# Kernel optimization log

Measured on AMD Instinct MI355X. Metric: run time of the kernel, lower is better.

The kernel has to match this reference:

```python
import jax, jax.numpy as jnp
import numpy as np

N_NODES = 50000
N_EDGES = 800000
IN_DIM = 128
HIDDEN = 128
NUM_CLASSES = 2
NUM_GRAPHS = 512


def _linear_params(key, fan_in, fan_out):
    # torch nn.Linear default init: U(-1/sqrt(fan_in), 1/sqrt(fan_in))
    k1, k2 = jax.random.split(key)
    bound = 1.0 / np.sqrt(fan_in)
    W = jax.random.uniform(k1, (fan_in, fan_out), jnp.float32, -bound, bound)
    b = jax.random.uniform(k2, (fan_out,), jnp.float32, -bound, bound)
    return W, b


def setup_inputs() -> dict:
    key = jax.random.key(0)
    ks = jax.random.split(key, 8)
    x = jax.random.normal(ks[0], (N_NODES, IN_DIM), jnp.float32)
    edge_index = jax.random.randint(ks[1], (2, N_EDGES), 0, N_NODES, jnp.int64)
    batch = jnp.sort(jax.random.randint(ks[2], (N_NODES,), 0, NUM_GRAPHS, jnp.int64))
    W1a, b1a = _linear_params(ks[3], IN_DIM, HIDDEN)
    W1b, b1b = _linear_params(ks[4], HIDDEN, HIDDEN)
    W2a, b2a = _linear_params(ks[5], HIDDEN, HIDDEN)
    W2b, b2b = _linear_params(ks[6], HIDDEN, HIDDEN)
    Wfc, bfc = _linear_params(ks[7], HIDDEN, NUM_CLASSES)
    return {"x": x, "edge_index": edge_index, "batch": batch,
            "W1a": W1a, "b1a": b1a, "W1b": W1b, "b1b": b1b,
            "W2a": W2a, "b2a": b2a, "W2b": W2b, "b2b": b2b,
            "Wfc": Wfc, "bfc": bfc}


def _gin_layer(x, src, dst, Wa, ba, Wb, bb):
    # GINConv (eps=0): h_i = MLP(x_i + sum_{j->i} x_j)
    agg = jax.ops.segment_sum(x[src], dst, num_segments=N_NODES)
    h = x + agg
    h = jax.nn.relu(h @ Wa + ba)
    h = h @ Wb + bb
    return jax.nn.relu(h)  # outer F.relu in forward; dropout is identity (eval)


def reference(x, edge_index, batch, W1a, b1a, W1b, b1b, W2a, b2a, W2b, b2b, Wfc, bfc):
    src, dst = edge_index[0], edge_index[1]
    h = _gin_layer(x, src, dst, W1a, b1a, W1b, b1b)
    h = _gin_layer(h, src, dst, W2a, b2a, W2b, b2b)
    # global mean pool per graph
    sums = jax.ops.segment_sum(h, batch, num_segments=NUM_GRAPHS)
    counts = jax.ops.segment_sum(jnp.ones((N_NODES,), h.dtype), batch, num_segments=NUM_GRAPHS)
    g_emb = sums / jnp.maximum(counts, 1.0)[:, None]
    return g_emb @ Wfc + bfc  # [NUM_GRAPHS, NUM_CLASSES]
```

## Files before the change

### kernel.cpp

```cpp
#include <hip/hip_runtime.h>

typedef unsigned short ushort_t;
typedef unsigned int uint_t;

typedef __bf16 bf16x8 __attribute__((ext_vector_type(8)));
typedef float f32x4 __attribute__((ext_vector_type(4)));

#define N_NODES 50000
#define N_EDGES 800000
#define DIM 128
#define NUM_GRAPHS 512
#define LDA 136

#define ELL_CAP 64

#define EDGE_GROUPS 8
#define EDGE_BUCKET ((N_NODES + EDGE_GROUPS - 1) / EDGE_GROUPS)
#define A_CHUNK 2048
#define A_BLOCKS ((N_EDGES + A_CHUNK - 1) / A_CHUNK)
#define FIFO_CAP 110592

#define PREP_X_BLOCKS 6250
#define PREP_W_BLOCKS 256
#define PREP_B_BLOCKS 196
#define PREP_TOTAL (A_BLOCKS + PREP_X_BLOCKS + PREP_W_BLOCKS + PREP_B_BLOCKS + 1)

#define SCATTER_BLOCKS 512

__device__ __forceinline__ float bf2f(ushort_t u) {
    return __uint_as_float(((uint_t)u) << 16);
}
__device__ __forceinline__ ushort_t f2bf(float f) {
    uint_t u = __float_as_uint(f);
    u = (u + 0x7FFF + ((u >> 16) & 1)) >> 16;
    return (ushort_t)u;
}
__device__ __forceinline__ bf16x8 as_bf16x8(uint4 v) {
    return __builtin_bit_cast(bf16x8, v);
}

__global__ void zero_detect_kernel(int* cnt, float* gsum, int* gcnt, const void* xraw,
                                   const void* eiraw, int* flags) {
    int i = blockIdx.x * 256 + threadIdx.x;
    if (i < N_NODES) cnt[i] = 0;
    if (i < NUM_GRAPHS * DIM) gsum[i] = 0.f;
    if (i < EDGE_GROUPS) gcnt[i] = 0;
    if (i == 0) {
        const ushort_t* u = (const ushort_t*)xraw;
        int extreme = 0;
        for (int k = 0; k < 128; ++k) {
            int e = (u[k] >> 7) & 0xFF;
            if (e >= 0xC0) extreme++;
        }
        flags[0] = (extreme > 8) ? 1 : 0;
        const int* p = (const int*)eiraw;
        int nonzero = 0;
        for (int k = 1; k < 64; k += 2) nonzero += (p[k] != 0);
        flags[1] = (nonzero == 0) ? 1 : 0;
    }
}

__global__ __launch_bounds__(256) void prep_all_kernel(
    const void* xraw, const void* braw, const void* eiraw,
    const void* W0, const void* W1, const void* W2, const void* W3,
    const void* pb1a, const void* pb1b, const void* pb2a, const void* pb2b,
    const void* pWfc, const void* pbfc, const int* __restrict__ flags,
    ushort_t* __restrict__ xout, ushort_t* __restrict__ wpout,
    int* __restrict__ batch32, float* __restrict__ params,
    int* __restrict__ gcnt, int2* __restrict__ fifo) {
    __shared__ int lcnt[EDGE_GROUPS];
    __shared__ int lbase[EDGE_GROUPS];
    int b = blockIdx.x;
    int tid = threadIdx.x;
    if (b < A_BLOCKS) {
        if (tid < EDGE_GROUPS) lcnt[tid] = 0;
        __syncthreads();
        const int* p = (const int*)eiraw;
        int i64 = flags[1];
        int base_e = b * A_CHUNK;
        int g[8], r[8], sv[8], dv[8];
#pragma unroll
        for (int k = 0; k < 8; ++k) {
            int e = base_e + k * 256 + tid;
            int valid = e < N_EDGES;
            int s = 0, d = 0;
            if (valid) {
                if (i64) { s = p[2 * e]; d = p[2 * (N_EDGES + e)]; }
                else     { s = p[e];     d = p[N_EDGES + e]; }
            }
            sv[k] = s; dv[k] = d;
            g[k] = valid ? (d / EDGE_BUCKET) : -1;
            r[k] = 0;
            if (valid) r[k] = atomicAdd(&lcnt[g[k]], 1);
        }
        __syncthreads();
        if (tid < EDGE_GROUPS) lbase[tid] = atomicAdd(&gcnt[tid], lcnt[tid]);
        __syncthreads();
#pragma unroll
        for (int k = 0; k < 8; ++k) {
            if (g[k] >= 0) {
                int pos = lbase[g[k]] + r[k];
                if (pos < FIFO_CAP)
                    fifo[(size_t)g[k] * FIFO_CAP + pos] = make_int2(sv[k], dv[k]);
            }
        }
    } else if (b < A_BLOCKS + PREP_X_BLOCKS) {
        if (flags[0]) {
            int i = (b - A_BLOCKS) * 256 + tid;
            if (i < N_NODES * DIM / 4) {
                float4 v = ((const float4*)xraw)[i];
                ushort4 o;
                o.x = f2bf(v.x); o.y = f2bf(v.y); o.z = f2bf(v.z); o.w = f2bf(v.w);
                ((ushort4*)xout)[i] = o;
            }
        }
    } else if (b < A_BLOCKS + PREP_X_BLOCKS + PREP_W_BLOCKS) {
        int gidx = (b - A_BLOCKS - PREP_X_BLOCKS) * 256 + tid;
        int which = gidx >> 14;
        const void* W = (which == 0) ? W0 : (which == 1) ? W1 : (which == 2) ? W2 : W3;
        int idx = gidx & 16383;
        int j = idx & 7;
        int L = (idx >> 3) & 63;
        int t = (idx >> 9) & 7;
        int s = idx >> 12;
        int k = s * 32 + (L >> 4) * 8 + j;
        int n = t * 16 + (L & 15);
        int off = k * DIM + n;
        wpout[gidx] = flags[0] ? f2bf(((const float*)W)[off]) : ((const ushort_t*)W)[off];
    } else if (b < A_BLOCKS + PREP_X_BLOCKS + PREP_W_BLOCKS + PREP_B_BLOCKS) {
        int i = (b - A_BLOCKS - PREP_X_BLOCKS - PREP_W_BLOCKS) * 256 + tid;
        if (i < N_NODES) {
            const int* p = (const int*)braw;
            batch32[i] = flags[1] ? p[2 * i] : p[i];
        }
    } else {
        for (int i = tid; i < 770; i += 256) {
            const void* srcp;
            int j;
            if (i < 128)      { srcp = pb1a; j = i; }
            else if (i < 256) { srcp = pb1b; j = i - 128; }
            else if (i < 384) { srcp = pb2a; j = i - 256; }
            else if (i < 512) { srcp = pb2b; j = i - 384; }
            else if (i < 768) { srcp = pWfc; j = i - 512; }
            else              { srcp = pbfc; j = i - 768; }
            params[i] = flags[0] ? ((const float*)srcp)[j] : bf2f(((const ushort_t*)srcp)[j]);
        }
    }
}

__global__ __launch_bounds__(256) void scatter_kernel(const int2* __restrict__ fifo,
                                                      const int* __restrict__ gcnt,
                                                      int* __restrict__ cnt,
                                                      int* __restrict__ ell) {
    int g = blockIdx.x & (EDGE_GROUPS - 1);
    int sub = blockIdx.x >> 3;
    int n = gcnt[g];
    if (n > FIFO_CAP) n = FIFO_CAP;
    const int2* f = fifo + (size_t)g * FIFO_CAP;
    for (int i = sub * 256 + threadIdx.x; i < n; i += (SCATTER_BLOCKS / EDGE_GROUPS) * 256) {
        int2 sd = f[i];
        int slot = atomicAdd(&cnt[sd.y], 1);
        if (slot < ELL_CAP) ell[sd.y * ELL_CAP + slot] = sd.x;
    }
}

__global__ __launch_bounds__(256) void agg_kernel(const ushort_t* __restrict__ featA,
                                                  const void* __restrict__ featB,
                                                  const int* __restrict__ flags,
                                                  const int* __restrict__ deg,
                                                  const int* __restrict__ ell,
                                                  ushort_t* __restrict__ hout) {
    int n = blockIdx.x * 16 + (threadIdx.x >> 4);
    int lane = threadIdx.x & 15;
    if (n >= N_NODES) return;
    const ushort_t* feat = featA;
    if (flags && !flags[0]) feat = (const ushort_t*)featB;
    const uint4* fp = reinterpret_cast<const uint4*>(feat);
    uint4 v = fp[(size_t)n * 16 + lane];
    float a0 = bf2f((ushort_t)(v.x & 0xffff));
    float a1 = bf2f((ushort_t)(v.x >> 16));
    float a2 = bf2f((ushort_t)(v.y & 0xffff));
    float a3 = bf2f((ushort_t)(v.y >> 16));
    float a4 = bf2f((ushort_t)(v.z & 0xffff));
    float a5 = bf2f((ushort_t)(v.z >> 16));
    float a6 = bf2f((ushort_t)(v.w & 0xffff));
    float a7 = bf2f((ushort_t)(v.w >> 16));
    int e1 = deg[n];
    if (e1 > ELL_CAP) e1 = ELL_CAP;
    const int4* __restrict__ rp4 = reinterpret_cast<const int4*>(ell + (size_t)n * ELL_CAP);
    const int* __restrict__ row = ell + (size_t)n * ELL_CAP;
    int j = 0;
#define ACC8(V) \
    a0 += bf2f((ushort_t)((V).x & 0xffff)); a1 += bf2f((ushort_t)((V).x >> 16)); \
    a2 += bf2f((ushort_t)((V).y & 0xffff)); a3 += bf2f((ushort_t)((V).y >> 16)); \
    a4 += bf2f((ushort_t)((V).z & 0xffff)); a5 += bf2f((ushort_t)((V).z >> 16)); \
    a6 += bf2f((ushort_t)((V).w & 0xffff)); a7 += bf2f((ushort_t)((V).w >> 16));
    for (; j + 8 <= e1; j += 8) {
        int4 ra = rp4[j >> 2];
        int4 rb = rp4[(j >> 2) + 1];
        uint4 g0 = fp[(size_t)ra.x * 16 + lane];
        uint4 g1 = fp[(size_t)ra.y * 16 + lane];
        uint4 g2 = fp[(size_t)ra.z * 16 + lane];
        uint4 g3 = fp[(size_t)ra.w * 16 + lane];
        uint4 g4 = fp[(size_t)rb.x * 16 + lane];
        uint4 g5 = fp[(size_t)rb.y * 16 + lane];
        uint4 g6 = fp[(size_t)rb.z * 16 + lane];
        uint4 g7 = fp[(size_t)rb.w * 16 + lane];
        ACC8(g0) ACC8(g1) ACC8(g2) ACC8(g3)
        ACC8(g4) ACC8(g5) ACC8(g6) ACC8(g7)
    }
    for (; j + 4 <= e1; j += 4) {
        int4 ra = rp4[j >> 2];
        uint4 g0 = fp[(size_t)ra.x * 16 + lane];
        uint4 g1 = fp[(size_t)ra.y * 16 + lane];
        uint4 g2 = fp[(size_t)ra.z * 16 + lane];
        uint4 g3 = fp[(size_t)ra.w * 16 + lane];
        ACC8(g0) ACC8(g1) ACC8(g2) ACC8(g3)
    }
    for (; j < e1; ++j) {
        int s = row[j];
        uint4 g0 = fp[(size_t)s * 16 + lane];
        ACC8(g0)
    }
#undef ACC8
    uint4 o;
    o.x = (uint_t)f2bf(a0) | ((uint_t)f2bf(a1) << 16);
    o.y = (uint_t)f2bf(a2) | ((uint_t)f2bf(a3) << 16);
    o.z = (uint_t)f2bf(a4) | ((uint_t)f2bf(a5) << 16);
    o.w = (uint_t)f2bf(a6) | ((uint_t)f2bf(a7) << 16);
    reinterpret_cast<uint4*>(hout)[(size_t)n * 16 + lane] = o;
}

__global__ __launch_bounds__(256) void mlp_kernel(const ushort_t* __restrict__ hin,
                                                  const ushort_t* __restrict__ wpA,
                                                  const float* __restrict__ ba,
                                                  const ushort_t* __restrict__ wpB,
                                                  const float* __restrict__ bb,
                                                  ushort_t* __restrict__ hout) {
    __shared__ ushort_t As[64 * LDA];
    int tid = threadIdx.x;
    int wave = tid >> 6;
    int lane = tid & 63;
    int quad = lane >> 4;
    int cl = lane & 15;
    int row0 = blockIdx.x * 64;

    bf16x8 B1[2][4], B2[2][4];
#pragma unroll
    for (int ti = 0; ti < 2; ++ti) {
        int t = 2 * wave + ti;
#pragma unroll
        for (int s = 0; s < 4; ++s) {
            B1[ti][s] = as_bf16x8(reinterpret_cast<const uint4*>(wpA)[(s * 8 + t) * 64 + lane]);
            B2[ti][s] = as_bf16x8(reinterpret_cast<const uint4*>(wpB)[(s * 8 + t) * 64 + lane]);
        }
    }

    for (int i = tid; i < 64 * 16; i += 256) {
        int r = i >> 4, c8 = i & 15;
        uint4 v = make_uint4(0u, 0u, 0u, 0u);
        int gr = row0 + r;
        if (gr < N_NODES)
            v = reinterpret_cast<const uint4*>(hin + (size_t)gr * DIM)[c8];
        *reinterpret_cast<uint4*>(&As[r * LDA + c8 * 8]) = v;
    }
    __syncthreads();

    f32x4 acc[4][2];
#pragma unroll
    for (int m = 0; m < 4; ++m)
#pragma unroll
        for (int ti = 0; ti < 2; ++ti)
#pragma unroll
            for (int r = 0; r < 4; ++r) acc[m][ti][r] = 0.f;

#pragma unroll
    for (int s = 0; s < 4; ++s) {
#pragma unroll
        for (int m = 0; m < 4; ++m) {
            bf16x8 a = *reinterpret_cast<const bf16x8*>(&As[(m * 16 + cl) * LDA + s * 32 + quad * 8]);
#pragma unroll
            for (int ti = 0; ti < 2; ++ti)
                acc[m][ti] = __builtin_amdgcn_mfma_f32_16x16x32_bf16(a, B1[ti][s], acc[m][ti], 0, 0, 0);
        }
    }
    __syncthreads();

#pragma unroll
    for (int ti = 0; ti < 2; ++ti) {
        int col = 32 * wave + ti * 16 + cl;
        float bv = ba[col];
#pragma unroll
        for (int m = 0; m < 4; ++m)
#pragma unroll
            for (int r = 0; r < 4; ++r) {
                float v = acc[m][ti][r] + bv;
                As[(m * 16 + quad * 4 + r) * LDA + col] = f2bf(fmaxf(v, 0.f));
            }
    }
    __syncthreads();

#pragma unroll
    for (int m = 0; m < 4; ++m)
#pragma unroll
        for (int ti = 0; ti < 2; ++ti)
#pragma unroll
            for (int r = 0; r < 4; ++r) acc[m][ti][r] = 0.f;

#pragma unroll
    for (int s = 0; s < 4; ++s) {
#pragma unroll
        for (int m = 0; m < 4; ++m) {
            bf16x8 a = *reinterpret_cast<const bf16x8*>(&As[(m * 16 + cl) * LDA + s * 32 + quad * 8]);
#pragma unroll
            for (int ti = 0; ti < 2; ++ti)
                acc[m][ti] = __builtin_amdgcn_mfma_f32_16x16x32_bf16(a, B2[ti][s], acc[m][ti], 0, 0, 0);
        }
    }

#pragma unroll
    for (int ti = 0; ti < 2; ++ti) {
        int col = 32 * wave + ti * 16 + cl;
        float bv = bb[col];
#pragma unroll
        for (int m = 0; m < 4; ++m)
#pragma unroll
            for (int r = 0; r < 4; ++r) {
                int gr = row0 + m * 16 + quad * 4 + r;
                if (gr < N_NODES) {
                    float v = acc[m][ti][r] + bv;
                    hout[(size_t)gr * DIM + col] = f2bf(fmaxf(v, 0.f));
                }
            }
    }
}

__global__ __launch_bounds__(256) void mlp_pool_kernel(const ushort_t* __restrict__ hin,
                                                       const ushort_t* __restrict__ wpA,
                                                       const float* __restrict__ ba,
                                                       const ushort_t* __restrict__ wpB,
                                                       const float* __restrict__ bb,
                                                       const int* __restrict__ batch32,
                                                       float* __restrict__ gsum) {
    __shared__ ushort_t As[64 * LDA];
    int tid = threadIdx.x;
    int wave = tid >> 6;
    int lane = tid & 63;
    int quad = lane >> 4;
    int cl = lane & 15;
    int row0 = blockIdx.x * 64;

    bf16x8 B1[2][4], B2[2][4];
#pragma unroll
    for (int ti = 0; ti < 2; ++ti) {
        int t = 2 * wave + ti;
#pragma unroll
        for (int s = 0; s < 4; ++s) {
            B1[ti][s] = as_bf16x8(reinterpret_cast<const uint4*>(wpA)[(s * 8 + t) * 64 + lane]);
            B2[ti][s] = as_bf16x8(reinterpret_cast<const uint4*>(wpB)[(s * 8 + t) * 64 + lane]);
        }
    }

    for (int i = tid; i < 64 * 16; i += 256) {
        int r = i >> 4, c8 = i & 15;
        uint4 v = make_uint4(0u, 0u, 0u, 0u);
        int gr = row0 + r;
        if (gr < N_NODES)
            v = reinterpret_cast<const uint4*>(hin + (size_t)gr * DIM)[c8];
        *reinterpret_cast<uint4*>(&As[r * LDA + c8 * 8]) = v;
    }
    __syncthreads();

    f32x4 acc[4][2];
#pragma unroll
    for (int m = 0; m < 4; ++m)
#pragma unroll
        for (int ti = 0; ti < 2; ++ti)
#pragma unroll
            for (int r = 0; r < 4; ++r) acc[m][ti][r] = 0.f;

#pragma unroll
    for (int s = 0; s < 4; ++s) {
#pragma unroll
        for (int m = 0; m < 4; ++m) {
            bf16x8 a = *reinterpret_cast<const bf16x8*>(&As[(m * 16 + cl) * LDA + s * 32 + quad * 8]);
#pragma unroll
            for (int ti = 0; ti < 2; ++ti)
                acc[m][ti] = __builtin_amdgcn_mfma_f32_16x16x32_bf16(a, B1[ti][s], acc[m][ti], 0, 0, 0);
        }
    }
    __syncthreads();

#pragma unroll
    for (int ti = 0; ti < 2; ++ti) {
        int col = 32 * wave + ti * 16 + cl;
        float bv = ba[col];
#pragma unroll
        for (int m = 0; m < 4; ++m)
#pragma unroll
            for (int r = 0; r < 4; ++r) {
                float v = acc[m][ti][r] + bv;
                As[(m * 16 + quad * 4 + r) * LDA + col] = f2bf(fmaxf(v, 0.f));
            }
    }
    __syncthreads();

#pragma unroll
    for (int m = 0; m < 4; ++m)
#pragma unroll
        for (int ti = 0; ti < 2; ++ti)
#pragma unroll
            for (int r = 0; r < 4; ++r) acc[m][ti][r] = 0.f;

#pragma unroll
    for (int s = 0; s < 4; ++s) {
#pragma unroll
        for (int m = 0; m < 4; ++m) {
            bf16x8 a = *reinterpret_cast<const bf16x8*>(&As[(m * 16 + cl) * LDA + s * 32 + quad * 8]);
#pragma unroll
            for (int ti = 0; ti < 2; ++ti)
                acc[m][ti] = __builtin_amdgcn_mfma_f32_16x16x32_bf16(a, B2[ti][s], acc[m][ti], 0, 0, 0);
        }
    }
    __syncthreads();

#pragma unroll
    for (int ti = 0; ti < 2; ++ti) {
        int col = 32 * wave + ti * 16 + cl;
        float bv = bb[col];
#pragma unroll
        for (int m = 0; m < 4; ++m)
#pragma unroll
            for (int r = 0; r < 4; ++r) {
                float v = acc[m][ti][r] + bv;
                As[(m * 16 + quad * 4 + r) * LDA + col] = f2bf(fmaxf(v, 0.f));
            }
    }
    __syncthreads();

    int c = tid & 127;
    int rbase = (tid >> 7) * 32;
    float accp = 0.f;
    int curg = -1;
    for (int r = rbase; r < rbase + 32; ++r) {
        int gr = row0 + r;
        if (gr >= N_NODES) break;
        int g = batch32[gr];
        if (g != curg) {
            if (curg >= 0) atomicAdd(&gsum[curg * DIM + c], accp);
            curg = g;
            accp = 0.f;
        }
        accp += bf2f(As[r * LDA + c]);
    }
    if (curg >= 0) atomicAdd(&gsum[curg * DIM + c], accp);
}

__global__ __launch_bounds__(64) void fc_kernel(const float* __restrict__ gsum,
                                                const int* __restrict__ batch,
                                                const float* __restrict__ params,
                                                const int* __restrict__ flags,
                                                void* __restrict__ out) {
    int g = blockIdx.x;
    int l = threadIdx.x;
    int lo = 0, hi = N_NODES;
    while (lo < hi) { int mid = (lo + hi) >> 1; if (batch[mid] < g) lo = mid + 1; else hi = mid; }
    int start = lo;
    hi = N_NODES;
    while (lo < hi) { int mid = (lo + hi) >> 1; if (batch[mid] < g + 1) lo = mid + 1; else hi = mid; }
    int cnt = lo - start;
    float inv = 1.0f / (float)(cnt > 0 ? cnt : 1);
    float m0 = gsum[g * DIM + l] * inv;
    float m1 = gsum[g * DIM + 64 + l] * inv;
    float p0 = m0 * params[512 + l * 2 + 0] + m1 * params[512 + (64 + l) * 2 + 0];
    float p1 = m0 * params[512 + l * 2 + 1] + m1 * params[512 + (64 + l) * 2 + 1];
#pragma unroll
    for (int off = 32; off > 0; off >>= 1) {
        p0 += __shfl_down(p0, off, 64);
        p1 += __shfl_down(p1, off, 64);
    }
    if (l == 0) {
        float o0 = p0 + params[768];
        float o1 = p1 + params[769];
        if (flags[0]) {
            ((float*)out)[g * 2 + 0] = o0;
            ((float*)out)[g * 2 + 1] = o1;
        } else {
            ((ushort_t*)out)[g * 2 + 0] = f2bf(o0);
            ((ushort_t*)out)[g * 2 + 1] = f2bf(o1);
        }
    }
}

extern "C" void kernel_launch(void* const* d_in, const int* in_sizes, int n_in,
                              void* d_out, int out_size, void* d_ws, size_t ws_size,
                              hipStream_t stream) {
    const void* x = d_in[0];
    const void* ei = d_in[1];
    const void* batch = d_in[2];
    const void* W1a = d_in[3];
    const void* b1a = d_in[4];
    const void* W1b = d_in[5];
    const void* b1b = d_in[6];
    const void* W2a = d_in[7];
    const void* b2a = d_in[8];
    const void* W2b = d_in[9];
    const void* b2b = d_in[10];
    const void* Wfc = d_in[11];
    const void* bfc = d_in[12];

    char* base = (char*)d_ws;
    ushort_t* hX = (ushort_t*)base;   base += (size_t)N_NODES * DIM * 2;
    ushort_t* hA = (ushort_t*)base;   base += (size_t)N_NODES * DIM * 2;
    int* ell = (int*)base;            base += (size_t)N_NODES * ELL_CAP * 4;
    int2* fifo = (int2*)base;         base += (size_t)EDGE_GROUPS * FIFO_CAP * 8;
    int* cnt = (int*)base;            base += (size_t)N_NODES * 4;
    int* batch32 = (int*)base;        base += (size_t)N_NODES * 4;
    int* gcnt = (int*)base;           base += 64;
    ushort_t* wp = (ushort_t*)base;   base += 4 * 16384 * 2;
    float* params = (float*)base;     base += 772 * 4;
    float* gsum = (float*)base;       base += (size_t)NUM_GRAPHS * DIM * 4;
    int* flags = (int*)base;          base += 16;

    ushort_t* wpA1 = wp;
    ushort_t* wpB1 = wp + 16384;
    ushort_t* wpA2 = wp + 2 * 16384;
    ushort_t* wpB2 = wp + 3 * 16384;

    zero_detect_kernel<<<256, 256, 0, stream>>>(cnt, gsum, gcnt, x, ei, flags);
    prep_all_kernel<<<PREP_TOTAL, 256, 0, stream>>>(x, batch, ei, W1a, W1b, W2a, W2b,
                                                    b1a, b1b, b2a, b2b, Wfc, bfc, flags,
                                                    hX, wp, batch32, params, gcnt, fifo);
    scatter_kernel<<<SCATTER_BLOCKS, 256, 0, stream>>>(fifo, gcnt, cnt, ell);

    agg_kernel<<<(N_NODES + 15) / 16, 256, 0, stream>>>(hX, x, flags, cnt, ell, hA);
    mlp_kernel<<<(N_NODES + 63) / 64, 256, 0, stream>>>(hA, wpA1, params + 0, wpB1, params + 128, hA);
    agg_kernel<<<(N_NODES + 15) / 16, 256, 0, stream>>>(hA, hA, nullptr, cnt, ell, hX);
    mlp_pool_kernel<<<(N_NODES + 63) / 64, 256, 0, stream>>>(hX, wpA2, params + 256, wpB2, params + 384,
                                                             batch32, gsum);
    fc_kernel<<<NUM_GRAPHS, 64, 0, stream>>>(gsum, batch32, params, flags, d_out);
}
```

Before: 247.5 us.

## Bucket edges into 256 fine destination ranges and build adjacency with shared-memory counters

Edges are partitioned into 256 buckets of 196 destination nodes each instead of 8 large groups, and each edge is packed into a single 32-bit word (16-bit source, 16-bit local destination). The scatter kernel now assigns one block per bucket and counts per-node degrees with shared-memory atomics, writing the count once per node, which removes global atomics on the degree array and the separate zeroing pass. This halves the size of the FIFO traffic but relies on source indices fitting in 16 bits, which holds for 50000 nodes. Each bucket's FIFO is capped at 4096 entries, against an average of about 3125 edges per bucket. The fine bucketing also adds more contention on the global bucket counters in the prep kernel.

```diff
diff --git a/kernel.cpp b/kernel.cpp
--- a/kernel.cpp
+++ b/kernel.cpp
@@ -14,19 +14,17 @@
 
 #define ELL_CAP 64
 
-#define EDGE_GROUPS 8
-#define EDGE_BUCKET ((N_NODES + EDGE_GROUPS - 1) / EDGE_GROUPS)
+#define NBUCK 256
+#define BUCK_SZ 196
+#define FIFO_CAP 4096
 #define A_CHUNK 2048
 #define A_BLOCKS ((N_EDGES + A_CHUNK - 1) / A_CHUNK)
-#define FIFO_CAP 110592
 
 #define PREP_X_BLOCKS 6250
 #define PREP_W_BLOCKS 256
 #define PREP_B_BLOCKS 196
 #define PREP_TOTAL (A_BLOCKS + PREP_X_BLOCKS + PREP_W_BLOCKS + PREP_B_BLOCKS + 1)
 
-#define SCATTER_BLOCKS 512
-
 __device__ __forceinline__ float bf2f(ushort_t u) {
     return __uint_as_float(((uint_t)u) << 16);
 }
@@ -39,12 +37,11 @@
     return __builtin_bit_cast(bf16x8, v);
 }
 
-__global__ void zero_detect_kernel(int* cnt, float* gsum, int* gcnt, const void* xraw,
+__global__ void zero_detect_kernel(float* gsum, int* gcnt, const void* xraw,
                                    const void* eiraw, int* flags) {
     int i = blockIdx.x * 256 + threadIdx.x;
-    if (i < N_NODES) cnt[i] = 0;
     if (i < NUM_GRAPHS * DIM) gsum[i] = 0.f;
-    if (i < EDGE_GROUPS) gcnt[i] = 0;
+    if (i < NBUCK) gcnt[i] = 0;
     if (i == 0) {
         const ushort_t* u = (const ushort_t*)xraw;
         int extreme = 0;
@@ -67,18 +64,19 @@
     const void* pWfc, const void* pbfc, const int* __restrict__ flags,
     ushort_t* __restrict__ xout, ushort_t* __restrict__ wpout,
     int* __restrict__ batch32, float* __restrict__ params,
-    int* __restrict__ gcnt, int2* __restrict__ fifo) {
-    __shared__ int lcnt[EDGE_GROUPS];
-    __shared__ int lbase[EDGE_GROUPS];
+    int* __restrict__ gcnt, uint_t* __restrict__ fifo) {
+    __shared__ int lcnt[NBUCK];
+    __shared__ int lbase[NBUCK];
     int b = blockIdx.x;
     int tid = threadIdx.x;
     if (b < A_BLOCKS) {
-        if (tid < EDGE_GROUPS) lcnt[tid] = 0;
+        lcnt[tid] = 0;
         __syncthreads();
         const int* p = (const int*)eiraw;
         int i64 = flags[1];
         int base_e = b * A_CHUNK;
-        int g[8], r[8], sv[8], dv[8];
+        int gk[8], rk[8];
+        uint_t pk[8];
 #pragma unroll
         for (int k = 0; k < 8; ++k) {
             int e = base_e + k * 256 + tid;
@@ -88,20 +86,20 @@
                 if (i64) { s = p[2 * e]; d = p[2 * (N_EDGES + e)]; }
                 else     { s = p[e];     d = p[N_EDGES + e]; }
             }
-            sv[k] = s; dv[k] = d;
-            g[k] = valid ? (d / EDGE_BUCKET) : -1;
-            r[k] = 0;
-            if (valid) r[k] = atomicAdd(&lcnt[g[k]], 1);
+            int g = d / BUCK_SZ;
+            gk[k] = valid ? g : -1;
+            pk[k] = (uint_t)s | ((uint_t)(d - g * BUCK_SZ) << 16);
+            rk[k] = valid ? atomicAdd(&lcnt[g], 1) : 0;
         }
         __syncthreads();
-        if (tid < EDGE_GROUPS) lbase[tid] = atomicAdd(&gcnt[tid], lcnt[tid]);
+        lbase[tid] = atomicAdd(&gcnt[tid], lcnt[tid]);
         __syncthreads();
 #pragma unroll
         for (int k = 0; k < 8; ++k) {
-            if (g[k] >= 0) {
-                int pos = lbase[g[k]] + r[k];
+            if (gk[k] >= 0) {
+                int pos = lbase[gk[k]] + rk[k];
                 if (pos < FIFO_CAP)
-                    fifo[(size_t)g[k] * FIFO_CAP + pos] = make_int2(sv[k], dv[k]);
+                    fifo[(size_t)gk[k] * FIFO_CAP + pos] = pk[k];
             }
         }
     } else if (b < A_BLOCKS + PREP_X_BLOCKS) {
@@ -148,19 +146,30 @@
     }
 }
 
-__global__ __launch_bounds__(256) void scatter_kernel(const int2* __restrict__ fifo,
+__global__ __launch_bounds__(256) void scatter_kernel(const uint_t* __restrict__ fifo,
                                                       const int* __restrict__ gcnt,
                                                       int* __restrict__ cnt,
                                                       int* __restrict__ ell) {
-    int g = blockIdx.x & (EDGE_GROUPS - 1);
-    int sub = blockIdx.x >> 3;
-    int n = gcnt[g];
+    __shared__ int lcnt[BUCK_SZ];
+    int b = blockIdx.x;
+    int tid = threadIdx.x;
+    if (tid < BUCK_SZ) lcnt[tid] = 0;
+    __syncthreads();
+    int n = gcnt[b];
     if (n > FIFO_CAP) n = FIFO_CAP;
-    const int2* f = fifo + (size_t)g * FIFO_CAP;
-    for (int i = sub * 256 + threadIdx.x; i < n; i += (SCATTER_BLOCKS / EDGE_GROUPS) * 256) {
-        int2 sd = f[i];
-        int slot = atomicAdd(&cnt[sd.y], 1);
-        if (slot < ELL_CAP) ell[sd.y * ELL_CAP + slot] = sd.x;
+    const uint_t* f = fifo + (size_t)b * FIFO_CAP;
+    int node0 = b * BUCK_SZ;
+    for (int i = tid; i < n; i += 256) {
+        uint_t e = f[i];
+        int s = (int)(e & 0xFFFFu);
+        int dl = (int)(e >> 16);
+        int slot = atomicAdd(&lcnt[dl], 1);
+        if (slot < ELL_CAP) ell[(size_t)(node0 + dl) * ELL_CAP + slot] = s;
+    }
+    __syncthreads();
+    if (tid < BUCK_SZ) {
+        int node = node0 + tid;
+        if (node < N_NODES) cnt[node] = lcnt[tid];
     }
 }
 
@@ -513,10 +522,10 @@
     ushort_t* hX = (ushort_t*)base;   base += (size_t)N_NODES * DIM * 2;
     ushort_t* hA = (ushort_t*)base;   base += (size_t)N_NODES * DIM * 2;
     int* ell = (int*)base;            base += (size_t)N_NODES * ELL_CAP * 4;
-    int2* fifo = (int2*)base;         base += (size_t)EDGE_GROUPS * FIFO_CAP * 8;
+    uint_t* fifo = (uint_t*)base;     base += (size_t)NBUCK * FIFO_CAP * 4;
     int* cnt = (int*)base;            base += (size_t)N_NODES * 4;
     int* batch32 = (int*)base;        base += (size_t)N_NODES * 4;
-    int* gcnt = (int*)base;           base += 64;
+    int* gcnt = (int*)base;           base += NBUCK * 4;
     ushort_t* wp = (ushort_t*)base;   base += 4 * 16384 * 2;
     float* params = (float*)base;     base += 772 * 4;
     float* gsum = (float*)base;       base += (size_t)NUM_GRAPHS * DIM * 4;
@@ -527,11 +536,11 @@
     ushort_t* wpA2 = wp + 2 * 16384;
     ushort_t* wpB2 = wp + 3 * 16384;
 
-    zero_detect_kernel<<<256, 256, 0, stream>>>(cnt, gsum, gcnt, x, ei, flags);
+    zero_detect_kernel<<<256, 256, 0, stream>>>(gsum, gcnt, x, ei, flags);
     prep_all_kernel<<<PREP_TOTAL, 256, 0, stream>>>(x, batch, ei, W1a, W1b, W2a, W2b,
                                                     b1a, b1b, b2a, b2b, Wfc, bfc, flags,
                                                     hX, wp, batch32, params, gcnt, fifo);
-    scatter_kernel<<<SCATTER_BLOCKS, 256, 0, stream>>>(fifo, gcnt, cnt, ell);
+    scatter_kernel<<<NBUCK, 256, 0, stream>>>(fifo, gcnt, cnt, ell);
 
     agg_kernel<<<(N_NODES + 15) / 16, 256, 0, stream>>>(hX, x, flags, cnt, ell, hA);
     mlp_kernel<<<(N_NODES + 63) / 64, 256, 0, stream>>>(hA, wpA1, params + 0, wpB1, params + 128, hA);
```

Result: faster. 228.2 us (-7.8%).
